# Kernel optimization log

Measured on AMD Instinct MI355X. Metric: run time of the kernel, lower is better.

## Reference

```python
import jax, jax.numpy as jnp
import numpy as np

DIM = 1024
HEADS = 16
D_HEAD = 64
INNER = HEADS * D_HEAD  # 1024
FF_INNER = 4 * DIM      # 4096


def setup_inputs() -> dict:
    key = jax.random.key(0)
    ks = jax.random.split(key, 12)
    s = lambda fan_in: 1.0 / np.sqrt(fan_in)
    x = jax.random.normal(ks[0], (4, 1024, DIM), dtype=jnp.float32)
    context = jax.random.normal(ks[1], (4, 2048, DIM), dtype=jnp.float32)
    Wq = jax.random.normal(ks[2], (DIM, INNER), dtype=jnp.float32) * s(DIM)
    Wk = jax.random.normal(ks[3], (DIM, INNER), dtype=jnp.float32) * s(DIM)
    Wv = jax.random.normal(ks[4], (DIM, INNER), dtype=jnp.float32) * s(DIM)
    Wo = jax.random.normal(ks[5], (INNER, DIM), dtype=jnp.float32) * s(INNER)
    bo = jax.random.normal(ks[6], (DIM,), dtype=jnp.float32) * 0.01
    W1 = jax.random.normal(ks[7], (DIM, FF_INNER), dtype=jnp.float32) * s(DIM)
    b1 = jax.random.normal(ks[8], (FF_INNER,), dtype=jnp.float32) * 0.01
    W2 = jax.random.normal(ks[9], (FF_INNER, DIM), dtype=jnp.float32) * s(FF_INNER)
    b2 = jax.random.normal(ks[10], (DIM,), dtype=jnp.float32) * 0.01
    return {"x": x, "context": context, "Wq": Wq, "Wk": Wk, "Wv": Wv,
            "Wo": Wo, "bo": bo, "W1": W1, "b1": b1, "W2": W2, "b2": b2}


def _block(x, context, Wq, Wk, Wv, Wo, bo, W1, b1, W2, b2):
    B, Lq, _ = x.shape
    scale = 1.0 / np.sqrt(D_HEAD).astype(np.float32)
    # cross attention
    q = (x @ Wq).reshape(B, Lq, HEADS, D_HEAD)          # [B,Lq,H,D]
    k = (context @ Wk).reshape(B, -1, HEADS, D_HEAD)    # [B,Lk,H,D]
    v = (context @ Wv).reshape(B, -1, HEADS, D_HEAD)
    sim = jnp.einsum('bqhd,bkhd->bhqk', q, k) * scale   # [B,H,Lq,Lk]
    attn = jax.nn.softmax(sim, axis=-1)
    out = jnp.einsum('bhqk,bkhd->bqhd', attn, v).reshape(B, Lq, INNER)
    x = out @ Wo + bo + x
    # feedforward (exact GELU as in torch F.gelu default)
    h = jax.nn.gelu(x @ W1 + b1, approximate=False)
    return h @ W2 + b2 + x


def reference(x, context, Wq, Wk, Wv, Wo, bo, W1, b1, W2, b2):
    return _block(x, context, Wq, Wk, Wv, Wo, bo, W1, b1, W2, b2)
```

## Files before the change

kernel.cpp:

```cpp
#include <hip/hip_runtime.h>
#include <cmath>
#include <cstdint>

typedef short s16x8 __attribute__((ext_vector_type(8)));
typedef float f32x4 __attribute__((ext_vector_type(4)));

__device__ __forceinline__ float bf2f(uint16_t u) {
  union { uint32_t i; float f; } c; c.i = ((uint32_t)u) << 16; return c.f;
}
__device__ __forceinline__ uint16_t f2bf(float f) {
  union { float f; uint32_t i; } c; c.f = f;
  return (uint16_t)((c.i + 0x7FFFu + ((c.i >> 16) & 1u)) >> 16);
}

__device__ __forceinline__ void gload16(const void* g, void* l) {
  __builtin_amdgcn_global_load_lds(
      (const __attribute__((address_space(1))) void*)g,
      (__attribute__((address_space(3))) void*)l, 16, 0, 0);
}

__device__ __forceinline__ bool sniff_is_bf16(const uint16_t* u16, int64_t n,
                                              int tid, int* s_cnt) {
  int cnt = 0;
#pragma unroll
  for (int j = 0; j < 4; j++) {
    int64_t idx = (((int64_t)(tid * 4 + j)) * 2) % n;
    idx &= ~(int64_t)1;
    uint32_t e = (u16[idx] >> 7) & 0xFF;
    cnt += (e >= 96 && e <= 144) ? 1 : 0;
  }
  if (tid == 0) *s_cnt = 0;
  __syncthreads();
  atomicAdd(s_cnt, cnt);
  __syncthreads();
  return (*s_cnt) * 10 > 1024 * 6;
}

__global__ __launch_bounds__(256) void zero_f32(float* __restrict__ p, int64_t n) {
  int64_t i = ((int64_t)blockIdx.x * 256 + threadIdx.x) * 4;
  if (i < n) *(f32x4*)(p + i) = (f32x4){0.f, 0.f, 0.f, 0.f};
}

__global__ __launch_bounds__(256) void convert_all(
    const void* xr, const void* cr, const void* bor, const void* b1r, const void* b2r,
    uint16_t* xo, uint16_t* co, uint16_t* boo, uint16_t* b1o, uint16_t* b2o) {
  __shared__ int s_cnt;
  const int id = blockIdx.x;
  const void* src; uint16_t* dst; int64_t tot; int64_t base; int n;
  if (id < 1024)      { src = xr;  dst = xo;  tot = 4194304; base = (int64_t)id * 4096;        n = 4096; }
  else if (id < 3072) { src = cr;  dst = co;  tot = 8388608; base = (int64_t)(id - 1024) * 4096; n = 4096; }
  else if (id == 3072){ src = bor; dst = boo; tot = 1024;    base = 0; n = 1024; }
  else if (id == 3073){ src = b1r; dst = b1o; tot = 4096;    base = 0; n = 4096; }
  else                { src = b2r; dst = b2o; tot = 1024;    base = 0; n = 1024; }
  const bool is16 = sniff_is_bf16((const uint16_t*)src, tot, threadIdx.x, &s_cnt);
  for (int i = threadIdx.x; i < n; i += 256) {
    const int64_t gi = base + i;
    dst[gi] = is16 ? ((const uint16_t*)src)[gi] : f2bf(((const float*)src)[gi]);
  }
}

__global__ __launch_bounds__(256) void transpose_all(
    const void* Wq, const void* Wk, const void* Wv, const void* Wo,
    const void* W1, const void* W2,
    uint16_t* WqT, uint16_t* WkT, uint16_t* WvT, uint16_t* WoT,
    uint16_t* W1T, uint16_t* W2T) {
  __shared__ int s_cnt;
  __shared__ uint16_t tile[32][34];
  const int id = blockIdx.x;
  const void* src; uint16_t* dst; int R, C, bx, by;
  if (id < 1024)      { src = Wq; dst = WqT; R = 1024; C = 1024; bx = id & 31;  by = id >> 5; }
  else if (id < 2048) { int t = id - 1024; src = Wk; dst = WkT; R = 1024; C = 1024; bx = t & 31; by = t >> 5; }
  else if (id < 3072) { int t = id - 2048; src = Wv; dst = WvT; R = 1024; C = 1024; bx = t & 31; by = t >> 5; }
  else if (id < 4096) { int t = id - 3072; src = Wo; dst = WoT; R = 1024; C = 1024; bx = t & 31; by = t >> 5; }
  else if (id < 8192) { int t = id - 4096; src = W1; dst = W1T; R = 1024; C = 4096; bx = t & 127; by = t >> 7; }
  else                { int t = id - 8192; src = W2; dst = W2T; R = 4096; C = 1024; bx = t & 31; by = t >> 5; }
  const uint16_t* u16 = (const uint16_t*)src;
  const float* f32 = (const float*)src;
  const bool is16 = sniff_is_bf16(u16, (int64_t)R * C, threadIdx.x, &s_cnt);

  const int tx = threadIdx.x & 31, ty = threadIdx.x >> 5;
  const int c0 = bx * 32, r0 = by * 32;
#pragma unroll
  for (int i = 0; i < 4; i++) {
    const int r = ty + i * 8;
    const int64_t gi = (int64_t)(r0 + r) * C + c0 + tx;
    tile[r][tx] = is16 ? u16[gi] : f2bf(f32[gi]);
  }
  __syncthreads();
#pragma unroll
  for (int i = 0; i < 4; i++) {
    const int r = ty + i * 8;
    dst[(int64_t)(c0 + r) * R + r0 + tx] = tile[tx][r];
  }
}

__global__ __launch_bounds__(256) void vtrans(
    const uint16_t* __restrict__ KVb, uint16_t* __restrict__ Vt) {
  __shared__ uint16_t tile[32][34];
  const int z = blockIdx.z;
  const uint16_t* in = KVb + (int64_t)z * 2048 * 2048 + 1024;
  uint16_t* out = Vt + (int64_t)z * 1024 * 2048;
  const int tx = threadIdx.x & 31, ty = threadIdx.x >> 5;
  const int c0 = blockIdx.x * 32, r0 = blockIdx.y * 32;
#pragma unroll
  for (int i = 0; i < 4; i++) {
    const int r = ty + i * 8;
    tile[r][tx] = in[(int64_t)(r0 + r) * 2048 + c0 + tx];
  }
  __syncthreads();
#pragma unroll
  for (int i = 0; i < 4; i++) {
    const int r = ty + i * 8;
    out[(int64_t)(c0 + r) * 2048 + r0 + tx] = tile[tx][r];
  }
}

#define BM 128
#define BN 128
#define BK 64

enum { EPI_NONE = 0, EPI_BIAS_RES = 1, EPI_BIAS_GELU = 2 };

template <int EPI, int RESF32, int OUTF32, int SPLITK>
__device__ __forceinline__ void gemm_body(
    const uint16_t* __restrict__ A, const uint16_t* __restrict__ Bt,
    void* __restrict__ Cv, const uint16_t* __restrict__ bias,
    const void* __restrict__ resid, int M, int N, int K_total,
    int m0, int n0, int zslice, uint16_t* As, uint16_t* Bs) {
  const int tid = threadIdx.x;
  const int w = tid >> 6, l = tid & 63;
  const int wu = __builtin_amdgcn_readfirstlane(w);
  const int wm = (w >> 1) * 64, wn = (w & 1) * 64;
  const int ls = l & 15, lg = l >> 4;
  const int K = SPLITK ? (K_total >> 1) : K_total;
  const int kof = SPLITK ? zslice * K : 0;

  const int sr = 8 * w + (l >> 3);
  const int koff = (((l & 7) ^ ((l >> 3) & 7)) * 8);
  const uint16_t* Ag = A + (int64_t)(m0 + sr) * K_total + kof + koff;
  const uint16_t* Bg = Bt + (int64_t)(n0 + sr) * K_total + kof + koff;
  const int64_t rstep = (int64_t)32 * K_total;

  uint16_t* lA = As + wu * 512;
  uint16_t* lB = Bs + wu * 512;

  f32x4 acc[4][4] = {};

  for (int kb = 0; kb < K; kb += BK) {
    __syncthreads();
#pragma unroll
    for (int r = 0; r < 4; r++) {
      gload16(Ag + r * rstep + kb, lA + r * 2048);
      gload16(Bg + r * rstep + kb, lB + r * 2048);
    }
    __syncthreads();
#pragma unroll
    for (int kk = 0; kk < 2; kk++) {
      s16x8 af[4], bfr[4];
#pragma unroll
      for (int i = 0; i < 4; i++) {
        const int row = wm + i * 16 + ls;
        af[i] = *(const s16x8*)&As[row * 64 + (((kk * 4 + lg) ^ (ls & 7)) * 8)];
      }
#pragma unroll
      for (int j = 0; j < 4; j++) {
        const int row = wn + j * 16 + ls;
        bfr[j] = *(const s16x8*)&Bs[row * 64 + (((kk * 4 + lg) ^ (ls & 7)) * 8)];
      }
#pragma unroll
      for (int i = 0; i < 4; i++)
#pragma unroll
        for (int j = 0; j < 4; j++)
          acc[i][j] = __builtin_amdgcn_mfma_f32_16x16x32_bf16(af[i], bfr[j], acc[i][j], 0, 0, 0);
    }
  }

#pragma unroll
  for (int i = 0; i < 4; i++) {
#pragma unroll
    for (int rr = 0; rr < 4; rr++) {
      const int64_t row = m0 + wm + i * 16 + lg * 4 + rr;
#pragma unroll
      for (int j = 0; j < 4; j++) {
        const int col = n0 + wn + j * 16 + ls;
        float v = acc[i][j][rr];
        if (EPI == EPI_BIAS_RES) {
          if (!SPLITK || zslice == 0) {
            const float rv = RESF32 ? ((const float*)resid)[row * N + col]
                                    : bf2f(((const uint16_t*)resid)[row * N + col]);
            v += bf2f(bias[col]) + rv;
          }
        } else if (EPI == EPI_BIAS_GELU) {
          v += bf2f(bias[col]);
          v = 0.5f * v * (1.0f + erff(v * 0.70710678118654752f));
        }
        if (SPLITK)
          atomicAdd((float*)Cv + row * N + col, v);
        else if (OUTF32)
          ((float*)Cv)[row * N + col] = v;
        else
          ((uint16_t*)Cv)[row * N + col] = f2bf(v);
      }
    }
  }
}

template <int EPI, int RESF32, int OUTF32, int SPLITK>
__global__ __launch_bounds__(256, 2) void gemm_single(
    const uint16_t* __restrict__ A, const uint16_t* __restrict__ Bt,
    void* __restrict__ Cv, const uint16_t* __restrict__ bias,
    const void* __restrict__ resid, int M, int N, int K_total) {
  __shared__ alignas(16) uint16_t As[BM * BK];
  __shared__ alignas(16) uint16_t Bs[BN * BK];
  gemm_body<EPI, RESF32, OUTF32, SPLITK>(A, Bt, Cv, bias, resid, M, N, K_total,
                                         blockIdx.x * BM, blockIdx.y * BN,
                                         (int)blockIdx.z, As, Bs);
}

__global__ __launch_bounds__(256, 2) void gemm_qkv(
    const uint16_t* __restrict__ xA, const uint16_t* __restrict__ WqT,
    uint16_t* __restrict__ Qb,
    const uint16_t* __restrict__ ctxA, const uint16_t* __restrict__ KVWt,
    uint16_t* __restrict__ KVb) {
  __shared__ alignas(16) uint16_t As[BM * BK];
  __shared__ alignas(16) uint16_t Bs[BN * BK];
  const int id = blockIdx.x;
  if (id < 256) {
    gemm_body<EPI_NONE, 0, 0, 0>(xA, WqT, Qb, nullptr, nullptr, 4096, 1024, 1024,
                                 (id & 31) * BM, (id >> 5) * BN, 0, As, Bs);
  } else {
    const int t = id - 256;
    gemm_body<EPI_NONE, 0, 0, 0>(ctxA, KVWt, KVb, nullptr, nullptr, 8192, 2048, 1024,
                                 (t & 63) * BM, (t >> 6) * BN, 0, As, Bs);
  }
}

#define KLD 72
#define PLD 72

__global__ __launch_bounds__(256, 2) void attn_kernel(
    const uint16_t* __restrict__ Q,
    const uint16_t* __restrict__ KV,
    const uint16_t* __restrict__ Vt,
    uint16_t* __restrict__ O) {
  __shared__ alignas(16) uint16_t Ks[64 * KLD];
  __shared__ alignas(16) uint16_t Vts[64 * KLD];
  __shared__ alignas(16) uint16_t Ps[8][16 * PLD];

  const int tid = threadIdx.x;
  const int w = tid >> 6, l = tid & 63;
  const int ls = l & 15, lg = l >> 4;

  const int blk = blockIdx.x;
  const int qb = blk & 7;
  const int h = (blk >> 3) & 15;
  const int b = blk >> 7;

  const int64_t qrow0 = (int64_t)b * 1024 + qb * 128;
  const int hoff = h * 64;
  const uint16_t* Vtb = Vt + (int64_t)b * 1024 * 2048;

  const float sc = 0.125f * 1.4426950408889634f;

  s16x8 qf[2][2];
#pragma unroll
  for (int qq = 0; qq < 2; qq++)
#pragma unroll
    for (int ks = 0; ks < 2; ks++) {
      s16x8 r = *(const s16x8*)(Q + (qrow0 + w * 32 + qq * 16 + ls) * 1024 + hoff + ks * 32 + lg * 8);
#pragma unroll
      for (int j = 0; j < 8; j++)
        qf[qq][ks][j] = (short)f2bf(bf2f((uint16_t)r[j]) * sc);
    }

  f32x4 oacc[2][4] = {};
  float lsum[2][4] = {};

  const int srow = tid >> 3;
  const int sc8 = (tid & 7) * 8;
  const uint16_t* Kg = KV + ((int64_t)b * 2048 + srow) * 2048 + hoff + sc8;
  const uint16_t* Vg = Vtb + (int64_t)(hoff + srow) * 2048 + sc8;

  s16x8 rk0 = *(const s16x8*)(Kg);
  s16x8 rk1 = *(const s16x8*)(Kg + (int64_t)32 * 2048);
  s16x8 rv0 = *(const s16x8*)(Vg);
  s16x8 rv1 = *(const s16x8*)(Vg + (int64_t)32 * 2048);

  for (int kt = 0; kt < 2048; kt += 64) {
    __syncthreads();
    *(s16x8*)&Ks[srow * KLD + sc8] = rk0;
    *(s16x8*)&Ks[(srow + 32) * KLD + sc8] = rk1;
    *(s16x8*)&Vts[srow * KLD + sc8] = rv0;
    *(s16x8*)&Vts[(srow + 32) * KLD + sc8] = rv1;
    const int ktn = kt + 64;
    if (ktn < 2048) {
      rk0 = *(const s16x8*)(Kg + (int64_t)ktn * 2048);
      rk1 = *(const s16x8*)(Kg + (int64_t)(ktn + 32) * 2048);
      rv0 = *(const s16x8*)(Vg + ktn);
      rv1 = *(const s16x8*)(Vg + ktn + (int64_t)32 * 2048);
    }
    __syncthreads();

    f32x4 s0[4], s1[4];
#pragma unroll
    for (int jn = 0; jn < 4; jn++) {
      f32x4 z = {0.f, 0.f, 0.f, 0.f};
      s0[jn] = z; s1[jn] = z;
#pragma unroll
      for (int ks = 0; ks < 2; ks++) {
        s16x8 kf = *(const s16x8*)&Ks[(jn * 16 + ls) * KLD + ks * 32 + lg * 8];
        s0[jn] = __builtin_amdgcn_mfma_f32_16x16x32_bf16(qf[0][ks], kf, s0[jn], 0, 0, 0);
        s1[jn] = __builtin_amdgcn_mfma_f32_16x16x32_bf16(qf[1][ks], kf, s1[jn], 0, 0, 0);
      }
    }

#pragma unroll
    for (int rr = 0; rr < 4; rr++) {
#pragma unroll
      for (int jn = 0; jn < 4; jn++) {
        const float p0 = exp2f(s0[jn][rr]);
        const float p1 = exp2f(s1[jn][rr]);
        Ps[w * 2 + 0][(lg * 4 + rr) * PLD + jn * 16 + ls] = f2bf(p0);
        Ps[w * 2 + 1][(lg * 4 + rr) * PLD + jn * 16 + ls] = f2bf(p1);
        lsum[0][rr] += p0;
        lsum[1][rr] += p1;
      }
    }

#pragma unroll
    for (int ks = 0; ks < 2; ks++) {
      s16x8 pf0 = *(const s16x8*)&Ps[w * 2 + 0][ls * PLD + ks * 32 + lg * 8];
      s16x8 pf1 = *(const s16x8*)&Ps[w * 2 + 1][ls * PLD + ks * 32 + lg * 8];
#pragma unroll
      for (int jn = 0; jn < 4; jn++) {
        s16x8 vf = *(const s16x8*)&Vts[(jn * 16 + ls) * KLD + ks * 32 + lg * 8];
        oacc[0][jn] = __builtin_amdgcn_mfma_f32_16x16x32_bf16(pf0, vf, oacc[0][jn], 0, 0, 0);
        oacc[1][jn] = __builtin_amdgcn_mfma_f32_16x16x32_bf16(pf1, vf, oacc[1][jn], 0, 0, 0);
      }
    }
  }

#pragma unroll
  for (int qq = 0; qq < 2; qq++)
#pragma unroll
    for (int rr = 0; rr < 4; rr++) {
      float red = lsum[qq][rr];
#pragma unroll
      for (int off = 1; off < 16; off <<= 1)
        red += __shfl_xor(red, off, 64);
      const float inv = 1.0f / red;
      const int64_t row = qrow0 + w * 32 + qq * 16 + lg * 4 + rr;
#pragma unroll
      for (int jn = 0; jn < 4; jn++)
        O[row * 1024 + hoff + jn * 16 + ls] = f2bf(oacc[qq][jn][rr] * inv);
    }
}

extern "C" void kernel_launch(void* const* d_in, const int* in_sizes, int n_in,
                              void* d_out, int out_size, void* d_ws, size_t ws_size,
                              hipStream_t stream) {
  const void* x_raw   = d_in[0];
  const void* ctx_raw = d_in[1];
  const void* Wq_raw  = d_in[2];
  const void* Wk_raw  = d_in[3];
  const void* Wv_raw  = d_in[4];
  const void* Wo_raw  = d_in[5];
  const void* bo_raw  = d_in[6];
  const void* W1_raw  = d_in[7];
  const void* b1_raw  = d_in[8];
  const void* W2_raw  = d_in[9];
  const void* b2_raw  = d_in[10];

  const int64_t Mi = 1 << 20;
  uint16_t* ws   = (uint16_t*)d_ws;
  uint16_t* WqT  = ws;
  uint16_t* KVWt = ws + 1 * Mi;
  uint16_t* WoT  = ws + 3 * Mi;
  uint16_t* W1T  = ws + 4 * Mi;
  uint16_t* W2T  = ws + 8 * Mi;
  uint16_t* bob  = ws + 12 * Mi;
  uint16_t* b1b  = ws + 12 * Mi + 1024;
  uint16_t* b2b  = ws + 12 * Mi + 5120;
  uint16_t* xb   = ws + 13 * Mi;
  uint16_t* AO   = ws + 13 * Mi;
  uint16_t* ctxb = ws + 17 * Mi;
  uint16_t* Vt   = ws + 17 * Mi;
  uint16_t* X1   = ws + 17 * Mi;
  uint16_t* Qb   = ws + 25 * Mi;
  uint16_t* KVb  = ws + 29 * Mi;
  uint16_t* Hb   = ws + 29 * Mi;

  const dim3 tb(256);
  zero_f32<<<dim3(4096), tb, 0, stream>>>((float*)d_out, (int64_t)4096 * 1024);
  convert_all<<<dim3(3075), tb, 0, stream>>>(x_raw, ctx_raw, bo_raw, b1_raw, b2_raw,
                                             xb, ctxb, bob, b1b, b2b);
  transpose_all<<<dim3(12288), tb, 0, stream>>>(Wq_raw, Wk_raw, Wv_raw, Wo_raw,
                                                W1_raw, W2_raw,
                                                WqT, KVWt, KVWt + Mi, WoT, W1T, W2T);

  gemm_qkv<<<dim3(1280), tb, 0, stream>>>(xb, WqT, Qb, ctxb, KVWt, KVb);

  vtrans<<<dim3(32, 64, 4), tb, 0, stream>>>(KVb, Vt);

  attn_kernel<<<dim3(512), tb, 0, stream>>>(Qb, KVb, Vt, AO);

  gemm_single<EPI_BIAS_RES, 1, 0, 0><<<dim3(32, 8), tb, 0, stream>>>(
      AO, WoT, X1, bob, x_raw, 4096, 1024, 1024);
  gemm_single<EPI_BIAS_GELU, 0, 0, 0><<<dim3(32, 32), tb, 0, stream>>>(
      X1, W1T, Hb, b1b, nullptr, 4096, 4096, 1024);
  gemm_single<EPI_BIAS_RES, 0, 1, 1><<<dim3(32, 8, 2), tb, 0, stream>>>(
      Hb, W2T, d_out, b2b, X1, 4096, 1024, 4096);
}
```

Baseline: 462.1 us.

## Restructure attention to 512 threads with one 16-row Q tile per wave

The attention kernel now runs 8 waves per block, each handling 16 query rows instead of 32. It computes S transposed (K as the A operand) so each lane writes packed bf16 probabilities to LDS. The block index mapping puts batch/head in the low bits and the row-sum reduction is reworked around the transposed layout. GEMM launch bounds rise from 2 to 3 blocks per CU, which may constrain registers and cause spills. The aim is more waves for latency hiding and fewer LDS stores, but each K/V tile is now reused by fewer MFMAs per wave.

```diff
diff --git a/kernel.cpp b/kernel.cpp
--- a/kernel.cpp
+++ b/kernel.cpp
@@ -1,4 +1,5 @@
 #include <hip/hip_runtime.h>
+#include <hip/hip_bf16.h>
 #include <cmath>
 #include <cstdint>
 
@@ -11,6 +12,11 @@
 __device__ __forceinline__ uint16_t f2bf(float f) {
   union { float f; uint32_t i; } c; c.f = f;
   return (uint16_t)((c.i + 0x7FFFu + ((c.i >> 16) & 1u)) >> 16);
+}
+__device__ __forceinline__ uint32_t pkbf(float a, float b) {
+  union { __hip_bfloat162 h; uint32_t u; } c;
+  c.h = __float22bfloat162_rn(float2{a, b});
+  return c.u;
 }
 
 __device__ __forceinline__ void gload16(const void* g, void* l) {
@@ -206,7 +212,7 @@
 }
 
 template <int EPI, int RESF32, int OUTF32, int SPLITK>
-__global__ __launch_bounds__(256, 2) void gemm_single(
+__global__ __launch_bounds__(256, 3) void gemm_single(
     const uint16_t* __restrict__ A, const uint16_t* __restrict__ Bt,
     void* __restrict__ Cv, const uint16_t* __restrict__ bias,
     const void* __restrict__ resid, int M, int N, int K_total) {
@@ -217,7 +223,7 @@
                                          (int)blockIdx.z, As, Bs);
 }
 
-__global__ __launch_bounds__(256, 2) void gemm_qkv(
+__global__ __launch_bounds__(256, 3) void gemm_qkv(
     const uint16_t* __restrict__ xA, const uint16_t* __restrict__ WqT,
     uint16_t* __restrict__ Qb,
     const uint16_t* __restrict__ ctxA, const uint16_t* __restrict__ KVWt,
@@ -238,7 +244,7 @@
 #define KLD 72
 #define PLD 72
 
-__global__ __launch_bounds__(256, 2) void attn_kernel(
+__global__ __launch_bounds__(512, 4) void attn_kernel(
     const uint16_t* __restrict__ Q,
     const uint16_t* __restrict__ KV,
     const uint16_t* __restrict__ Vt,
@@ -252,9 +258,9 @@
   const int ls = l & 15, lg = l >> 4;
 
   const int blk = blockIdx.x;
-  const int qb = blk & 7;
-  const int h = (blk >> 3) & 15;
-  const int b = blk >> 7;
+  const int bh = blk & 63;
+  const int qb = blk >> 6;
+  const int h = bh & 15, b = bh >> 4;
 
   const int64_t qrow0 = (int64_t)b * 1024 + qb * 128;
   const int hoff = h * 64;
@@ -262,98 +268,83 @@
 
   const float sc = 0.125f * 1.4426950408889634f;
 
-  s16x8 qf[2][2];
-#pragma unroll
-  for (int qq = 0; qq < 2; qq++)
-#pragma unroll
-    for (int ks = 0; ks < 2; ks++) {
-      s16x8 r = *(const s16x8*)(Q + (qrow0 + w * 32 + qq * 16 + ls) * 1024 + hoff + ks * 32 + lg * 8);
-#pragma unroll
-      for (int j = 0; j < 8; j++)
-        qf[qq][ks][j] = (short)f2bf(bf2f((uint16_t)r[j]) * sc);
-    }
-
-  f32x4 oacc[2][4] = {};
-  float lsum[2][4] = {};
+  s16x8 qf[2];
+#pragma unroll
+  for (int ks = 0; ks < 2; ks++) {
+    s16x8 r = *(const s16x8*)(Q + (qrow0 + w * 16 + ls) * 1024 + hoff + ks * 32 + lg * 8);
+#pragma unroll
+    for (int j = 0; j < 8; j++)
+      qf[ks][j] = (short)f2bf(bf2f((uint16_t)r[j]) * sc);
+  }
+
+  f32x4 oacc[4] = {};
+  float lsum = 0.f;
 
   const int srow = tid >> 3;
   const int sc8 = (tid & 7) * 8;
   const uint16_t* Kg = KV + ((int64_t)b * 2048 + srow) * 2048 + hoff + sc8;
   const uint16_t* Vg = Vtb + (int64_t)(hoff + srow) * 2048 + sc8;
 
-  s16x8 rk0 = *(const s16x8*)(Kg);
-  s16x8 rk1 = *(const s16x8*)(Kg + (int64_t)32 * 2048);
-  s16x8 rv0 = *(const s16x8*)(Vg);
-  s16x8 rv1 = *(const s16x8*)(Vg + (int64_t)32 * 2048);
+  s16x8 rk = *(const s16x8*)(Kg);
+  s16x8 rv = *(const s16x8*)(Vg);
 
   for (int kt = 0; kt < 2048; kt += 64) {
     __syncthreads();
-    *(s16x8*)&Ks[srow * KLD + sc8] = rk0;
-    *(s16x8*)&Ks[(srow + 32) * KLD + sc8] = rk1;
-    *(s16x8*)&Vts[srow * KLD + sc8] = rv0;
-    *(s16x8*)&Vts[(srow + 32) * KLD + sc8] = rv1;
+    *(s16x8*)&Ks[srow * KLD + sc8] = rk;
+    *(s16x8*)&Vts[srow * KLD + sc8] = rv;
     const int ktn = kt + 64;
     if (ktn < 2048) {
-      rk0 = *(const s16x8*)(Kg + (int64_t)ktn * 2048);
-      rk1 = *(const s16x8*)(Kg + (int64_t)(ktn + 32) * 2048);
-      rv0 = *(const s16x8*)(Vg + ktn);
-      rv1 = *(const s16x8*)(Vg + ktn + (int64_t)32 * 2048);
+      rk = *(const s16x8*)(Kg + (int64_t)ktn * 2048);
+      rv = *(const s16x8*)(Vg + ktn);
     }
     __syncthreads();
 
-    f32x4 s0[4], s1[4];
+    f32x4 st[4];
 #pragma unroll
     for (int jn = 0; jn < 4; jn++) {
       f32x4 z = {0.f, 0.f, 0.f, 0.f};
-      s0[jn] = z; s1[jn] = z;
+      st[jn] = z;
 #pragma unroll
       for (int ks = 0; ks < 2; ks++) {
         s16x8 kf = *(const s16x8*)&Ks[(jn * 16 + ls) * KLD + ks * 32 + lg * 8];
-        s0[jn] = __builtin_amdgcn_mfma_f32_16x16x32_bf16(qf[0][ks], kf, s0[jn], 0, 0, 0);
-        s1[jn] = __builtin_amdgcn_mfma_f32_16x16x32_bf16(qf[1][ks], kf, s1[jn], 0, 0, 0);
+        st[jn] = __builtin_amdgcn_mfma_f32_16x16x32_bf16(kf, qf[ks], st[jn], 0, 0, 0);
       }
     }
 
 #pragma unroll
-    for (int rr = 0; rr < 4; rr++) {
-#pragma unroll
-      for (int jn = 0; jn < 4; jn++) {
-        const float p0 = exp2f(s0[jn][rr]);
-        const float p1 = exp2f(s1[jn][rr]);
-        Ps[w * 2 + 0][(lg * 4 + rr) * PLD + jn * 16 + ls] = f2bf(p0);
-        Ps[w * 2 + 1][(lg * 4 + rr) * PLD + jn * 16 + ls] = f2bf(p1);
-        lsum[0][rr] += p0;
-        lsum[1][rr] += p1;
-      }
+    for (int jn = 0; jn < 4; jn++) {
+      const float p0 = exp2f(st[jn][0]);
+      const float p1 = exp2f(st[jn][1]);
+      const float p2 = exp2f(st[jn][2]);
+      const float p3 = exp2f(st[jn][3]);
+      lsum += (p0 + p1) + (p2 + p3);
+      uint2 pk; pk.x = pkbf(p0, p1); pk.y = pkbf(p2, p3);
+      *(uint2*)&Ps[w][ls * PLD + jn * 16 + lg * 4] = pk;
     }
 
 #pragma unroll
     for (int ks = 0; ks < 2; ks++) {
-      s16x8 pf0 = *(const s16x8*)&Ps[w * 2 + 0][ls * PLD + ks * 32 + lg * 8];
-      s16x8 pf1 = *(const s16x8*)&Ps[w * 2 + 1][ls * PLD + ks * 32 + lg * 8];
+      s16x8 pf = *(const s16x8*)&Ps[w][ls * PLD + ks * 32 + lg * 8];
 #pragma unroll
       for (int jn = 0; jn < 4; jn++) {
         s16x8 vf = *(const s16x8*)&Vts[(jn * 16 + ls) * KLD + ks * 32 + lg * 8];
-        oacc[0][jn] = __builtin_amdgcn_mfma_f32_16x16x32_bf16(pf0, vf, oacc[0][jn], 0, 0, 0);
-        oacc[1][jn] = __builtin_amdgcn_mfma_f32_16x16x32_bf16(pf1, vf, oacc[1][jn], 0, 0, 0);
+        oacc[jn] = __builtin_amdgcn_mfma_f32_16x16x32_bf16(pf, vf, oacc[jn], 0, 0, 0);
       }
     }
   }
 
-#pragma unroll
-  for (int qq = 0; qq < 2; qq++)
-#pragma unroll
-    for (int rr = 0; rr < 4; rr++) {
-      float red = lsum[qq][rr];
-#pragma unroll
-      for (int off = 1; off < 16; off <<= 1)
-        red += __shfl_xor(red, off, 64);
-      const float inv = 1.0f / red;
-      const int64_t row = qrow0 + w * 32 + qq * 16 + lg * 4 + rr;
-#pragma unroll
-      for (int jn = 0; jn < 4; jn++)
-        O[row * 1024 + hoff + jn * 16 + ls] = f2bf(oacc[qq][jn][rr] * inv);
-    }
+  float red = lsum;
+  red += __shfl_xor(red, 16, 64);
+  red += __shfl_xor(red, 32, 64);
+
+#pragma unroll
+  for (int rr = 0; rr < 4; rr++) {
+    const float inv = 1.0f / __shfl(red, lg * 4 + rr, 64);
+    const int64_t row = qrow0 + w * 16 + lg * 4 + rr;
+#pragma unroll
+    for (int jn = 0; jn < 4; jn++)
+      O[row * 1024 + hoff + jn * 16 + ls] = f2bf(oacc[jn][rr] * inv);
+  }
 }
 
 extern "C" void kernel_launch(void* const* d_in, const int* in_sizes, int n_in,
@@ -402,7 +393,7 @@
 
   vtrans<<<dim3(32, 64, 4), tb, 0, stream>>>(KVb, Vt);
 
-  attn_kernel<<<dim3(512), tb, 0, stream>>>(Qb, KVb, Vt, AO);
+  attn_kernel<<<dim3(512), dim3(512), 0, stream>>>(Qb, KVb, Vt, AO);
 
   gemm_single<EPI_BIAS_RES, 1, 0, 0><<<dim3(32, 8), tb, 0, stream>>>(
       AO, WoT, X1, bob, x_raw, 4096, 1024, 1024);
```

After: 436.9 us. 1.06x faster.
